# Performance work log

Measured on AMD Instinct MI355X. Metric: run time of the kernel, lower is better.

The kernel has to match this reference:

```python
import jax, jax.numpy as jnp
import numpy as np

K = 3          # kernel_size
A = 4          # spatial_atoms
PAD = (K - 1) // 2


def _unfold(x, k, pad):
    # torch F.unfold equivalent -> (B, C, k*k, H, W), taps ordered (kh, kw)
    B, C, H, W = x.shape
    xp = jnp.pad(x, ((0, 0), (0, 0), (pad, pad), (pad, pad)))
    taps = [xp[:, :, i:i + H, j:j + W] for i in range(k) for j in range(k)]
    return jnp.stack(taps, axis=2)


def setup_inputs() -> dict:
    key = jax.random.key(0)
    k1, k2, k3, k4 = jax.random.split(key, 4)
    B, C, O, H, W = 8, 64, 64, 64, 64
    x = jax.random.normal(k1, (B, C, H, W), dtype=jnp.float32)
    w_gen = jax.random.normal(k2, (O * A * K * K, C), dtype=jnp.float32) * 0.05
    b_gen = jax.random.normal(k3, (O * A * K * K,), dtype=jnp.float32) * 0.05
    pos_enc = jax.random.uniform(k4, (A, 2), dtype=jnp.float32, minval=-1.0, maxval=1.0)
    return {"x": x, "w_gen": w_gen, "b_gen": b_gen, "pos_enc": pos_enc}


def reference(x, w_gen, b_gen, pos_enc):
    B, C, H, W = x.shape
    O = w_gen.shape[0] // (A * K * K)

    # filter_gen: 1x1 conv + ReLU -> (B, O*A*K*K, H, W)
    filters = jnp.einsum('bchw,fc->bfhw', x, w_gen) + b_gen[None, :, None, None]
    filters = jax.nn.relu(filters)
    filters = filters.reshape(B, O, A, K * K, H, W)

    # position grid: stack((x_grid, y_grid)) with meshgrid indexing='ij'
    ys = jnp.linspace(-1.0, 1.0, H)
    xs = jnp.linspace(-1.0, 1.0, W)
    grid = jnp.stack(jnp.meshgrid(xs, ys, indexing='xy'), axis=-1)  # (H, W, 2)

    # spatial attention: (A, H, W)
    diff = grid[None] - pos_enc[:, None, None, :]
    att = jnp.exp(-jnp.sum(diff * diff, axis=-1))

    # combine atoms: (B, O, K*K, H, W)
    combined = jnp.einsum('boakhw,ahw->bokhw', filters, att)

    # unfold input and weighted sum over taps (valid since C == O)
    patches = _unfold(x, K, PAD)  # (B, C, K*K, H, W)
    out = jnp.sum(combined * patches, axis=2)  # (B, O, H, W)
    return out
```

## Files before the change

### kernel.cpp

```cpp
#include <hip/hip_runtime.h>
#include <math.h>

constexpr int NB = 8, NC = 64, NO = 64, NH = 64, NW = 64;

using f32x4 = __attribute__((ext_vector_type(4))) float;
using s16x8 = __attribute__((ext_vector_type(8))) short;
using u32x4 = __attribute__((ext_vector_type(4))) unsigned int;

__device__ __forceinline__ unsigned int pk2(float lo, float hi) {
    unsigned int r;
    asm("v_cvt_pk_bf16_f32 %0, %1, %2" : "=v"(r) : "v"(lo), "v"(hi));
    return r;
}
__device__ __forceinline__ unsigned short f2bf(float f) {
    unsigned u = __builtin_bit_cast(unsigned, f);
    return (unsigned short)((u + 0x7fffu + ((u >> 16) & 1u)) >> 16);
}
__device__ __forceinline__ float bf2f(unsigned short s) {
    unsigned u = ((unsigned)s) << 16;
    return __builtin_bit_cast(float, u);
}

__global__ __launch_bounds__(1024, 1)
void acda_kernel(const float* __restrict__ x, const float* __restrict__ w_gen,
                 const float* __restrict__ b_gen, const float* __restrict__ pos_enc,
                 float* __restrict__ out)
{
    __shared__ __align__(16) unsigned char arena[65536];
    __shared__ unsigned short Ws[16 * 36 * 64];
    __shared__ float BiasL[36 * 16];

    const int tid  = threadIdx.x;
    const int lane = tid & 63;
    const int wv   = tid >> 6;
    const int c0   = lane & 15, q = lane >> 4;
    const int hrow = wv >> 1, whalf = wv & 1;

    const int bx    = blockIdx.x;
    const int osub  = bx & 3;
    const int hoct  = (bx >> 2) & 7;
    const int b     = bx >> 5;
    const int hbase = hoct * 8;
    const int obase = osub * 16;
    const size_t xB = (size_t)b * NC * NH * NW;

    for (int u = tid; u < 4608; u += 1024) {
        const int o_l = u / 288;
        const int r   = u - o_l * 288;
        const int t   = r >> 3, cseg = r & 7;
        const float* src = w_gen + ((size_t)(obase + o_l) * 36 + t) * NC + cseg * 8;
        const float4 v0 = *reinterpret_cast<const float4*>(src);
        const float4 v1 = *reinterpret_cast<const float4*>(src + 4);
        u32x4 pk;
        pk[0] = pk2(v0.x, v0.y); pk[1] = pk2(v0.z, v0.w);
        pk[2] = pk2(v1.x, v1.y); pk[3] = pk2(v1.z, v1.w);
        const int byte = (o_l * 36 + t) * 128 + ((cseg * 16) ^ ((o_l & 7) << 4));
        *reinterpret_cast<u32x4*>(reinterpret_cast<char*>(Ws) + byte) = pk;
    }
    {
        const int w = lane;
#pragma unroll
        for (int i = 0; i < 4; ++i) {
            const int pair = wv * 4 + i;
            const int hs = pair >> 3, oct = pair & 7;
            const float* src = x + xB + (size_t)(oct * 8) * (NH * NW) + (hbase + hs) * NW + w;
            u32x4 pkv;
#pragma unroll
            for (int j = 0; j < 4; ++j)
                pkv[j] = pk2(src[(size_t)(2 * j) * (NH * NW)], src[(size_t)(2 * j + 1) * (NH * NW)]);
            const int loc  = hs * 64 + w;
            const int byte = loc * 128 + ((oct * 16) ^ ((loc & 7) << 4));
            *reinterpret_cast<u32x4*>(arena + byte) = pkv;
        }
    }
    for (int i = tid; i < 576; i += 1024) {
        const int t = i >> 4, o_l = i & 15;
        BiasL[i] = b_gen[(obase + o_l) * 36 + t];
    }
    __syncthreads();

    s16x8 xf[2][2];
#pragma unroll
    for (int nt = 0; nt < 2; ++nt) {
        const int loc = hrow * 64 + whalf * 32 + nt * 16 + c0;
#pragma unroll
        for (int kh2 = 0; kh2 < 2; ++kh2) {
            const int byte = loc * 128 + ((kh2 * 64 + q * 16) ^ ((loc & 7) << 4));
            xf[nt][kh2] = *reinterpret_cast<s16x8*>(arena + byte);
        }
    }
    __syncthreads();

    unsigned short* Patch = reinterpret_cast<unsigned short*>(arena);
    {
        const int o_l = tid >> 6, w = tid & 63;
        const float* xo = x + xB + (size_t)(obase + o_l) * (NH * NW);
#pragma unroll
        for (int hhi = 0; hhi < 10; ++hhi) {
            const int hh = hbase - 1 + hhi;
            const float v = (hh >= 0 && hh < NH) ? xo[hh * NW + w] : 0.0f;
            Patch[(hhi * 66 + w + 1) * 20 + o_l] = f2bf(v);
            if (w < 2) Patch[(hhi * 66 + (w ? 65 : 0)) * 20 + o_l] = 0;
        }
    }
    __syncthreads();

    const float gy = -1.0f + (2.0f / 63.0f) * (float)(hbase + hrow);
    float gxn[2];
#pragma unroll
    for (int nt = 0; nt < 2; ++nt)
        gxn[nt] = -1.0f + (2.0f / 63.0f) * (float)(whalf * 32 + nt * 16 + c0);

    const int wswz = (c0 & 7) << 4;
    const char* wrowp = reinterpret_cast<const char*>(Ws) + c0 * (36 * 128);

    float outacc[2][4] = {};

#pragma unroll
    for (int a = 0; a < 4; ++a) {
        float attn[2];
#pragma unroll
        for (int nt = 0; nt < 2; ++nt) {
            const float dx = gxn[nt] - pos_enc[2 * a], dy = gy - pos_enc[2 * a + 1];
            attn[nt] = __expf(-(dx * dx + dy * dy));
        }
#pragma unroll
        for (int k = 0; k < 9; ++k) {
            const int t  = a * 9 + k;
            const int kh = k / 3, kw = k - 3 * kh;
            const s16x8 wf0 = *reinterpret_cast<const s16x8*>(wrowp + t * 128 + ((q * 16) ^ wswz));
            const s16x8 wf1 = *reinterpret_cast<const s16x8*>(wrowp + t * 128 + ((64 + q * 16) ^ wswz));
            const f32x4 bb  = *reinterpret_cast<const f32x4*>(BiasL + t * 16 + q * 4);
#pragma unroll
            for (int nt = 0; nt < 2; ++nt) {
                f32x4 acc = bb;
                acc = __builtin_amdgcn_mfma_f32_16x16x32_bf16(wf0, xf[nt][0], acc, 0, 0, 0);
                acc = __builtin_amdgcn_mfma_f32_16x16x32_bf16(wf1, xf[nt][1], acc, 0, 0, 0);
                const ushort4 pu = *reinterpret_cast<const ushort4*>(
                    reinterpret_cast<const char*>(Patch) +
                    (((hrow + kh) * 66 + whalf * 32 + nt * 16 + c0 + kw) * 20 + q * 4) * 2);
                const float at = attn[nt];
                outacc[nt][0] = fmaf(fmaxf(acc[0], 0.f) * at, bf2f(pu.x), outacc[nt][0]);
                outacc[nt][1] = fmaf(fmaxf(acc[1], 0.f) * at, bf2f(pu.y), outacc[nt][1]);
                outacc[nt][2] = fmaf(fmaxf(acc[2], 0.f) * at, bf2f(pu.z), outacc[nt][2]);
                outacc[nt][3] = fmaf(fmaxf(acc[3], 0.f) * at, bf2f(pu.w), outacc[nt][3]);
            }
        }
    }

    const int h = hbase + hrow;
#pragma unroll
    for (int nt = 0; nt < 2; ++nt) {
        const int wcol = whalf * 32 + nt * 16 + c0;
#pragma unroll
        for (int r = 0; r < 4; ++r) {
            const int o = obase + q * 4 + r;
            out[(((size_t)b * NO + o) * NH + h) * NW + wcol] = outacc[nt][r];
        }
    }
}

extern "C" void kernel_launch(void* const* d_in, const int* in_sizes, int n_in,
                              void* d_out, int out_size, void* d_ws, size_t ws_size,
                              hipStream_t stream) {
    const float* x       = (const float*)d_in[0];
    const float* w_gen   = (const float*)d_in[1];
    const float* b_gen   = (const float*)d_in[2];
    const float* pos_enc = (const float*)d_in[3];
    float* out = (float*)d_out;

    dim3 grid(NB * 8 * 4);
    dim3 block(1024);
    hipLaunchKernelGGL(acda_kernel, grid, block, 0, stream,
                       x, w_gen, b_gen, pos_enc, out);
}
```

Baseline: 26.22 us.

## Halve block size, give each wave a full row, reorder loops tap-major

Blocks shrink from 1024 to 512 threads, and each wave now covers a full 64-wide row, four 16-column tiles, instead of half a row. Each weight and bias LDS fragment is therefore reused across four MFMA tiles instead of two. The loop nest is reordered so the sum over atoms happens in registers per tap before the patch multiply, which cuts patch LDS reads by a factor of four. Attention values are precomputed once, and the patch fill uses float2 loads. The cost is higher register pressure and fewer waves per block, which may hurt latency hiding with 256 blocks.

```diff
diff --git a/kernel.cpp b/kernel.cpp
--- a/kernel.cpp
+++ b/kernel.cpp
@@ -21,7 +21,7 @@
     return __builtin_bit_cast(float, u);
 }
 
-__global__ __launch_bounds__(1024, 1)
+__global__ __launch_bounds__(512, 1)
 void acda_kernel(const float* __restrict__ x, const float* __restrict__ w_gen,
                  const float* __restrict__ b_gen, const float* __restrict__ pos_enc,
                  float* __restrict__ out)
@@ -34,7 +34,7 @@
     const int lane = tid & 63;
     const int wv   = tid >> 6;
     const int c0   = lane & 15, q = lane >> 4;
-    const int hrow = wv >> 1, whalf = wv & 1;
+    const int hrow = wv;
 
     const int bx    = blockIdx.x;
     const int osub  = bx & 3;
@@ -44,7 +44,7 @@
     const int obase = osub * 16;
     const size_t xB = (size_t)b * NC * NH * NW;
 
-    for (int u = tid; u < 4608; u += 1024) {
+    for (int u = tid; u < 4608; u += 512) {
         const int o_l = u / 288;
         const int r   = u - o_l * 288;
         const int t   = r >> 3, cseg = r & 7;
@@ -60,8 +60,8 @@
     {
         const int w = lane;
 #pragma unroll
-        for (int i = 0; i < 4; ++i) {
-            const int pair = wv * 4 + i;
+        for (int i = 0; i < 8; ++i) {
+            const int pair = wv * 8 + i;
             const int hs = pair >> 3, oct = pair & 7;
             const float* src = x + xB + (size_t)(oct * 8) * (NH * NW) + (hbase + hs) * NW + w;
             u32x4 pkv;
@@ -73,16 +73,16 @@
             *reinterpret_cast<u32x4*>(arena + byte) = pkv;
         }
     }
-    for (int i = tid; i < 576; i += 1024) {
+    for (int i = tid; i < 576; i += 512) {
         const int t = i >> 4, o_l = i & 15;
         BiasL[i] = b_gen[(obase + o_l) * 36 + t];
     }
     __syncthreads();
 
-    s16x8 xf[2][2];
+    s16x8 xf[4][2];
 #pragma unroll
-    for (int nt = 0; nt < 2; ++nt) {
-        const int loc = hrow * 64 + whalf * 32 + nt * 16 + c0;
+    for (int nt = 0; nt < 4; ++nt) {
+        const int loc = hrow * 64 + nt * 16 + c0;
 #pragma unroll
         for (int kh2 = 0; kh2 < 2; ++kh2) {
             const int byte = loc * 128 + ((kh2 * 64 + q * 16) ^ ((loc & 7) << 4));
@@ -93,65 +93,78 @@
 
     unsigned short* Patch = reinterpret_cast<unsigned short*>(arena);
     {
-        const int o_l = tid >> 6, w = tid & 63;
+        const int o_l = tid >> 5, w2 = (tid & 31) * 2;
         const float* xo = x + xB + (size_t)(obase + o_l) * (NH * NW);
 #pragma unroll
         for (int hhi = 0; hhi < 10; ++hhi) {
             const int hh = hbase - 1 + hhi;
-            const float v = (hh >= 0 && hh < NH) ? xo[hh * NW + w] : 0.0f;
-            Patch[(hhi * 66 + w + 1) * 20 + o_l] = f2bf(v);
-            if (w < 2) Patch[(hhi * 66 + (w ? 65 : 0)) * 20 + o_l] = 0;
+            float2 v = {0.f, 0.f};
+            if (hh >= 0 && hh < NH) v = *reinterpret_cast<const float2*>(xo + hh * NW + w2);
+            Patch[(hhi * 66 + w2 + 1) * 20 + o_l] = f2bf(v.x);
+            Patch[(hhi * 66 + w2 + 2) * 20 + o_l] = f2bf(v.y);
         }
+    }
+    if (tid < 320) {
+        const int hhi = tid >> 5, side = (tid >> 4) & 1, o_l = tid & 15;
+        Patch[(hhi * 66 + (side ? 65 : 0)) * 20 + o_l] = 0;
     }
     __syncthreads();
 
     const float gy = -1.0f + (2.0f / 63.0f) * (float)(hbase + hrow);
-    float gxn[2];
+    float attv[4][4];
 #pragma unroll
-    for (int nt = 0; nt < 2; ++nt)
-        gxn[nt] = -1.0f + (2.0f / 63.0f) * (float)(whalf * 32 + nt * 16 + c0);
+    for (int a = 0; a < 4; ++a) {
+        const float px = pos_enc[2 * a], py = pos_enc[2 * a + 1];
+#pragma unroll
+        for (int nt = 0; nt < 4; ++nt) {
+            const float gx = -1.0f + (2.0f / 63.0f) * (float)(nt * 16 + c0);
+            const float dx = gx - px, dy = gy - py;
+            attv[a][nt] = __expf(-(dx * dx + dy * dy));
+        }
+    }
 
     const int wswz = (c0 & 7) << 4;
     const char* wrowp = reinterpret_cast<const char*>(Ws) + c0 * (36 * 128);
 
-    float outacc[2][4] = {};
+    float outacc[4][4] = {};
 
 #pragma unroll
-    for (int a = 0; a < 4; ++a) {
-        float attn[2];
+    for (int k = 0; k < 9; ++k) {
+        float tsum[4][4] = {};
 #pragma unroll
-        for (int nt = 0; nt < 2; ++nt) {
-            const float dx = gxn[nt] - pos_enc[2 * a], dy = gy - pos_enc[2 * a + 1];
-            attn[nt] = __expf(-(dx * dx + dy * dy));
-        }
-#pragma unroll
-        for (int k = 0; k < 9; ++k) {
-            const int t  = a * 9 + k;
-            const int kh = k / 3, kw = k - 3 * kh;
+        for (int a = 0; a < 4; ++a) {
+            const int t = a * 9 + k;
             const s16x8 wf0 = *reinterpret_cast<const s16x8*>(wrowp + t * 128 + ((q * 16) ^ wswz));
             const s16x8 wf1 = *reinterpret_cast<const s16x8*>(wrowp + t * 128 + ((64 + q * 16) ^ wswz));
             const f32x4 bb  = *reinterpret_cast<const f32x4*>(BiasL + t * 16 + q * 4);
 #pragma unroll
-            for (int nt = 0; nt < 2; ++nt) {
+            for (int nt = 0; nt < 4; ++nt) {
                 f32x4 acc = bb;
                 acc = __builtin_amdgcn_mfma_f32_16x16x32_bf16(wf0, xf[nt][0], acc, 0, 0, 0);
                 acc = __builtin_amdgcn_mfma_f32_16x16x32_bf16(wf1, xf[nt][1], acc, 0, 0, 0);
-                const ushort4 pu = *reinterpret_cast<const ushort4*>(
-                    reinterpret_cast<const char*>(Patch) +
-                    (((hrow + kh) * 66 + whalf * 32 + nt * 16 + c0 + kw) * 20 + q * 4) * 2);
-                const float at = attn[nt];
-                outacc[nt][0] = fmaf(fmaxf(acc[0], 0.f) * at, bf2f(pu.x), outacc[nt][0]);
-                outacc[nt][1] = fmaf(fmaxf(acc[1], 0.f) * at, bf2f(pu.y), outacc[nt][1]);
-                outacc[nt][2] = fmaf(fmaxf(acc[2], 0.f) * at, bf2f(pu.z), outacc[nt][2]);
-                outacc[nt][3] = fmaf(fmaxf(acc[3], 0.f) * at, bf2f(pu.w), outacc[nt][3]);
+                const float at = attv[a][nt];
+#pragma unroll
+                for (int r = 0; r < 4; ++r)
+                    tsum[nt][r] = fmaf(at, fmaxf(acc[r], 0.f), tsum[nt][r]);
             }
+        }
+        const int kh = k / 3, kw = k - 3 * kh;
+#pragma unroll
+        for (int nt = 0; nt < 4; ++nt) {
+            const ushort4 pu = *reinterpret_cast<const ushort4*>(
+                reinterpret_cast<const char*>(Patch) +
+                (((hrow + kh) * 66 + nt * 16 + c0 + kw) * 20 + q * 4) * 2);
+            outacc[nt][0] = fmaf(tsum[nt][0], bf2f(pu.x), outacc[nt][0]);
+            outacc[nt][1] = fmaf(tsum[nt][1], bf2f(pu.y), outacc[nt][1]);
+            outacc[nt][2] = fmaf(tsum[nt][2], bf2f(pu.z), outacc[nt][2]);
+            outacc[nt][3] = fmaf(tsum[nt][3], bf2f(pu.w), outacc[nt][3]);
         }
     }
 
     const int h = hbase + hrow;
 #pragma unroll
-    for (int nt = 0; nt < 2; ++nt) {
-        const int wcol = whalf * 32 + nt * 16 + c0;
+    for (int nt = 0; nt < 4; ++nt) {
+        const int wcol = nt * 16 + c0;
 #pragma unroll
         for (int r = 0; r < 4; ++r) {
             const int o = obase + q * 4 + r;
@@ -170,7 +183,7 @@
     float* out = (float*)d_out;
 
     dim3 grid(NB * 8 * 4);
-    dim3 block(1024);
+    dim3 block(512);
     hipLaunchKernelGGL(acda_kernel, grid, block, 0, stream,
                        x, w_gen, b_gen, pos_enc, out);
 }
```

New measurement: 25.88 us. Within noise of the previous version (-1.3%).
